# Optimization experiments

Hardware: AMD Instinct MI355X
Metric: run time of the kernel (lower is better)

Reference implementation:

```python
import jax, jax.numpy as jnp
import numpy as np

N_NODES = 50000
N_EDGES = 800000
D_IN = 128
D_OUT = 128


def setup_inputs() -> dict:
    key = jax.random.key(0)
    k1, k2, k3, k4, k5 = jax.random.split(key, 5)
    x = jax.random.normal(k1, (N_NODES, D_IN), dtype=jnp.float32)
    # fc weight, torch Linear convention: [out_dim, in_dim]
    W = jax.random.normal(k2, (D_OUT, D_IN), dtype=jnp.float32) * (1.0 / np.sqrt(D_IN))
    # attn_fc weight: [1, 2*out_dim], no bias
    a = jax.random.normal(k3, (1, 2 * D_OUT), dtype=jnp.float32) * (1.0 / np.sqrt(2 * D_OUT))
    src = jax.random.randint(k4, (N_EDGES,), 0, N_NODES)
    dst = jax.random.randint(k5, (N_EDGES,), 0, N_NODES)
    return {"x": x, "W": W, "a": a, "src": src, "dst": dst}


def reference(x, W, a, src, dst):
    # h = fc(x)
    h = x @ W.T  # [N, D_OUT]
    # attn_fc(cat([h_src, h_dst])) == h_src @ a[:D] + h_dst @ a[D:] (linear, no bias),
    # so precompute per-node scalars instead of materializing [E, 2*D_OUT].
    a_src = a[0, :D_OUT]
    a_dst = a[0, D_OUT:]
    s = h @ a_src  # [N]
    d = h @ a_dst  # [N]
    e = jax.nn.sigmoid(s[src] + d[dst])[:, None]  # [E, 1]
    msg = e * h[src]  # [E, D_OUT]  edge gather + weight
    # reduce: f[v] = sum over incoming edges of e * h_src
    f = jax.ops.segment_sum(msg, dst, num_segments=N_NODES)  # [N, D_OUT]
    return f
```

## Files before the change

### kernel.cpp

```cpp
#include <hip/hip_runtime.h>
#include <hip/hip_bf16.h>
#include <stdint.h>

#define NN 50000
#define NE 800000
#define DD 128
#define NBKT 3125
#define BCH 4096
#define BGRID ((NE + BCH - 1) / BCH)
#define CAP 384
#define SPILL_CAP 32768
#define GROWS 64
#define GGRID ((NN + GROWS - 1) / GROWS)
#define NSEG 4

typedef __attribute__((ext_vector_type(8))) unsigned short ushort8;
typedef __attribute__((ext_vector_type(8))) short short8;
typedef __attribute__((ext_vector_type(4))) float f32x4;

__device__ inline uint32_t cvtpk(float lo, float hi) {
    uint32_t r;
    asm("v_cvt_pk_bf16_f32 %0, %1, %2" : "=v"(r) : "v"(lo), "v"(hi));
    return r;
}
__device__ inline float bf_lo(uint32_t u) { return __uint_as_float(u << 16); }
__device__ inline float bf_hi(uint32_t u) { return __uint_as_float(u & 0xffff0000u); }

__global__ __launch_bounds__(256) void prep_k(const float* __restrict__ W,
                                              uint16_t* __restrict__ Wb,
                                              int* __restrict__ cntg) {
    int t = threadIdx.x;
    if (blockIdx.x < 13) {
        for (int k = blockIdx.x * 256 + t; k < NBKT + 4; k += 13 * 256) cntg[k] = 0;
    }
    int i = blockIdx.x * 256 + t;
    if (i < DD * DD) {
        uint32_t u = __float_as_uint(W[i]);
        Wb[i] = (uint16_t)((u + 0x7fffu + ((u >> 16) & 1u)) >> 16);
    }
}

__global__ __launch_bounds__(256) void fused_k(const float* __restrict__ x,
                                               const uint16_t* __restrict__ Wb,
                                               const float* __restrict__ a,
                                               const int* __restrict__ src,
                                               const int* __restrict__ dst,
                                               uint16_t* __restrict__ hb,
                                               float* __restrict__ sArr,
                                               float* __restrict__ dArr,
                                               int* __restrict__ cntg,
                                               int* __restrict__ scnt,
                                               uint32_t* __restrict__ rec,
                                               uint2* __restrict__ spill) {
    __shared__ int lh[NBKT];
    __shared__ int gb[NBKT];
    const int t = threadIdx.x;

    if ((int)blockIdx.x < GGRID) {
        const int l = t & 63, wid = t >> 6;
        const int r0 = blockIdx.x * GROWS;
        const int lr = l & 15, lk = l >> 4;

        f32x4 acc[8];
        #pragma unroll
        for (int c = 0; c < 8; ++c) acc[c] = f32x4{0.f, 0.f, 0.f, 0.f};

        const int arow = r0 + wid * 16 + lr;
        const int lrow = (arow < NN) ? arow : (NN - 1);
        const float* xp = x + (size_t)lrow * DD + lk * 8;

        #pragma unroll
        for (int kc = 0; kc < 4; ++kc) {
            float4 v0 = *(const float4*)(xp + kc * 32);
            float4 v1 = *(const float4*)(xp + kc * 32 + 4);
            union { uint32_t u[4]; short8 s; } A;
            A.u[0] = cvtpk(v0.x, v0.y); A.u[1] = cvtpk(v0.z, v0.w);
            A.u[2] = cvtpk(v1.x, v1.y); A.u[3] = cvtpk(v1.z, v1.w);
            #pragma unroll
            for (int c = 0; c < 8; ++c) {
                int col = c * 16 + lr;
                short8 bf_ = *(const short8*)(Wb + (size_t)col * DD + kc * 32 + lk * 8);
                acc[c] = __builtin_amdgcn_mfma_f32_16x16x32_bf16(A.s, bf_, acc[c], 0, 0, 0);
            }
        }

        float avs[8], avd[8];
        #pragma unroll
        for (int c = 0; c < 8; ++c) {
            avs[c] = a[c * 16 + lr];
            avd[c] = a[DD + c * 16 + lr];
        }
        #pragma unroll
        for (int i = 0; i < 4; ++i) {
            float ps = 0.f, pd = 0.f;
            #pragma unroll
            for (int c = 0; c < 8; ++c) {
                ps = fmaf(acc[c][i], avs[c], ps);
                pd = fmaf(acc[c][i], avd[c], pd);
            }
            #pragma unroll
            for (int o = 8; o > 0; o >>= 1) {
                ps += __shfl_xor(ps, o);
                pd += __shfl_xor(pd, o);
            }
            int row = r0 + wid * 16 + lk * 4 + i;
            if (lr == 0 && row < NN) { sArr[row] = ps; dArr[row] = pd; }
        }

        #pragma unroll
        for (int i = 0; i < 4; ++i) {
            int row = r0 + wid * 16 + lk * 4 + i;
            if (row < NN) {
                union { uint32_t u[4]; ushort8 s; } H;
                H.u[0] = cvtpk(acc[0][i], acc[1][i]);
                H.u[1] = cvtpk(acc[2][i], acc[3][i]);
                H.u[2] = cvtpk(acc[4][i], acc[5][i]);
                H.u[3] = cvtpk(acc[6][i], acc[7][i]);
                *(ushort8*)(hb + (size_t)row * DD + lr * 8) = H.s;
            }
        }
    } else {
        int bb = blockIdx.x - GGRID;
        for (int k = t; k < NBKT; k += 256) lh[k] = 0;
        __syncthreads();
        int base = bb * BCH;
        unsigned pk[16]; int bk[16];
        #pragma unroll
        for (int i = 0; i < 16; ++i) {
            int idx = base + i * 256 + t;
            if (idx < NE) {
                int s_ = src[idx], d_ = dst[idx];
                bk[i] = d_ >> 4;
                pk[i] = ((unsigned)(d_ & 15) << 16) | (unsigned)s_;
                atomicAdd(&lh[bk[i]], 1);
            } else bk[i] = -1;
        }
        __syncthreads();
        for (int k = t; k < NBKT; k += 256) {
            int c = lh[k];
            lh[k] = 0;
            gb[k] = c ? atomicAdd(&cntg[k], c) : 0;
        }
        __syncthreads();
        #pragma unroll
        for (int i = 0; i < 16; ++i) {
            if (bk[i] >= 0) {
                int sl = atomicAdd(&lh[bk[i]], 1);
                int p = gb[bk[i]] + sl;
                if (p < CAP) {
                    rec[(size_t)bk[i] * CAP + p] = pk[i];
                } else {
                    int sp = atomicAdd(scnt, 1);
                    if (sp < SPILL_CAP)
                        spill[sp] = make_uint2(pk[i] & 0xffffu,
                                               (unsigned)(bk[i] * 16 + (int)(pk[i] >> 16)));
                }
            }
        }
    }
}

__global__ __launch_bounds__(256) void bsort_agg_k(const uint16_t* __restrict__ hb,
                                                   const float* __restrict__ sA,
                                                   const float* __restrict__ dA,
                                                   const int* __restrict__ cntg,
                                                   const uint32_t* __restrict__ rec,
                                                   const int* __restrict__ scnt,
                                                   const uint2* __restrict__ spill,
                                                   float* __restrict__ out) {
    __shared__ uint32_t srt[CAP];
    __shared__ float    eL[CAP];
    __shared__ float dAl[16];
    __shared__ int hbin[NSEG * 16];
    __shared__ int soff[NSEG * 16 + 1];
    __shared__ int curw[NSEG * 16];
    int t = threadIdx.x, l = t & 63, wid = t >> 6;
    int b = blockIdx.x;
    int cnt = cntg[b]; if (cnt > CAP) cnt = CAP;
    int beg = b * CAP;
    int n0 = b * 16;
    int ns = *scnt; if (ns > SPILL_CAP) ns = SPILL_CAP;
    if (t < 64) hbin[t] = 0;
    if (t < 16) dAl[t] = dA[n0 + t];
    __syncthreads();

    uint32_t rc[2]; float er[2]; int bn[2]; int nrc = 0;
    for (int j = t; j < cnt; j += 256) {
        uint32_t r = rec[beg + j];
        int sv = (int)(r & 0xffffu);
        int sg = (sv >= 12500) + (sv >= 25000) + (sv >= 37500);
        int bin = (sg << 4) | (int)(r >> 16);
        rc[nrc] = r; bn[nrc] = bin;
        atomicAdd(&hbin[bin], 1);
        float z = sA[sv] + dAl[r >> 16];
        er[nrc] = 1.f / (1.f + __expf(-z));
        ++nrc;
    }
    __syncthreads();
    if (wid == 0) {
        int v = hbin[l];
        int inc = v;
        #pragma unroll
        for (int o = 1; o < 64; o <<= 1) {
            int nb = __shfl_up(inc, o);
            if (l >= o) inc += nb;
        }
        soff[l + 1] = inc;
        if (l == 0) soff[0] = 0;
        curw[l] = inc - v;
    }
    __syncthreads();
    for (int k = 0; k < nrc; ++k) {
        int p = atomicAdd(&curw[bn[k]], 1);
        srt[p] = rc[k];
        eL[p] = er[k];
    }
    __syncthreads();

    const int q = l >> 4, sl = l & 15;
    const int d = wid * 4 + q;
    const int n = n0 + d;
    const char* hbp = (const char*)hb;
    const int s0 = (blockIdx.x & 7) >> 1;
    float acc[8] = {0.f,0.f,0.f,0.f,0.f,0.f,0.f,0.f};

    #pragma unroll
    for (int so = 0; so < NSEG; ++so) {
        int s = (s0 + so) & (NSEG - 1);
        int bin = (s << 4) | d;
        int js = soff[bin], je = soff[bin + 1];
        for (int j = js; j < je; j += 2) {
            int j1 = j + 1;
            bool v1 = j1 < je;
            uint32_t r0 = srt[j];
            uint32_t r1 = srt[v1 ? j1 : j];
            float e0 = eL[j];
            float e1 = v1 ? eL[j1] : 0.f;
            uint4 u0 = *(const uint4*)(hbp + (size_t)(r0 & 0xffffu) * 256 + sl * 16);
            uint4 u1 = *(const uint4*)(hbp + (size_t)(r1 & 0xffffu) * 256 + sl * 16);
            acc[0] = fmaf(e0, bf_lo(u0.x), acc[0]); acc[1] = fmaf(e0, bf_hi(u0.x), acc[1]);
            acc[2] = fmaf(e0, bf_lo(u0.y), acc[2]); acc[3] = fmaf(e0, bf_hi(u0.y), acc[3]);
            acc[4] = fmaf(e0, bf_lo(u0.z), acc[4]); acc[5] = fmaf(e0, bf_hi(u0.z), acc[5]);
            acc[6] = fmaf(e0, bf_lo(u0.w), acc[6]); acc[7] = fmaf(e0, bf_hi(u0.w), acc[7]);
            acc[0] = fmaf(e1, bf_lo(u1.x), acc[0]); acc[1] = fmaf(e1, bf_hi(u1.x), acc[1]);
            acc[2] = fmaf(e1, bf_lo(u1.y), acc[2]); acc[3] = fmaf(e1, bf_hi(u1.y), acc[3]);
            acc[4] = fmaf(e1, bf_lo(u1.z), acc[4]); acc[5] = fmaf(e1, bf_hi(u1.z), acc[5]);
            acc[6] = fmaf(e1, bf_lo(u1.w), acc[6]); acc[7] = fmaf(e1, bf_hi(u1.w), acc[7]);
        }
    }

    if (ns > 0) {
        for (int i = 0; i < ns; ++i) {
            uint2 sp = spill[i];
            if ((int)sp.y == n) {
                float z = sA[sp.x] + dAl[d];
                float e = 1.f / (1.f + __expf(-z));
                uint4 u = *(const uint4*)(hbp + (size_t)sp.x * 256 + sl * 16);
                acc[0] = fmaf(e, bf_lo(u.x), acc[0]); acc[1] = fmaf(e, bf_hi(u.x), acc[1]);
                acc[2] = fmaf(e, bf_lo(u.y), acc[2]); acc[3] = fmaf(e, bf_hi(u.y), acc[3]);
                acc[4] = fmaf(e, bf_lo(u.z), acc[4]); acc[5] = fmaf(e, bf_hi(u.z), acc[5]);
                acc[6] = fmaf(e, bf_lo(u.w), acc[6]); acc[7] = fmaf(e, bf_hi(u.w), acc[7]);
            }
        }
    }

    float* orow = out + (size_t)n * DD;
    #pragma unroll
    for (int k = 0; k < 8; ++k) orow[k * 16 + sl] = acc[k];
}

__global__ __launch_bounds__(256) void edge_atomic_k(const int* __restrict__ src, const int* __restrict__ dst,
                                                     const float* __restrict__ sArr, const float* __restrict__ dArr,
                                                     const uint32_t* __restrict__ hb, float* __restrict__ out) {
    int wid = threadIdx.x >> 6, l = threadIdx.x & 63;
    int e = blockIdx.x * 4 + wid;
    if (e >= NE) return;
    int sv = src[e], dv = dst[e];
    float z = sArr[sv] + dArr[dv];
    float ev = 1.0f / (1.0f + __expf(-z));
    uint32_t u = hb[(size_t)sv * 64 + l];
    int colx = 32 * (l & 3) + (l >> 2);
    atomicAdd(&out[(size_t)dv * DD + colx],      ev * bf_lo(u));
    atomicAdd(&out[(size_t)dv * DD + colx + 16], ev * bf_hi(u));
}

extern "C" void kernel_launch(void* const* d_in, const int* in_sizes, int n_in,
                              void* d_out, int out_size, void* d_ws, size_t ws_size,
                              hipStream_t stream) {
    const float* x  = (const float*)d_in[0];
    const float* W  = (const float*)d_in[1];
    const float* a  = (const float*)d_in[2];
    const int* src  = (const int*)d_in[3];
    const int* dst  = (const int*)d_in[4];
    float* out = (float*)d_out;

    char* p = (char*)d_ws;
    uint16_t* hb = (uint16_t*)p;            p += (size_t)NN * DD * 2;
    uint16_t* Wb = (uint16_t*)p;            p += (size_t)DD * DD * 2;
    float* sA    = (float*)p;               p += (size_t)NN * 4;
    float* dA    = (float*)p;               p += (size_t)NN * 4;
    int*   cntg  = (int*)p;                 p += (size_t)NBKT * 4;
    int*   scnt  = (int*)p;                 p += 16;
    uint32_t* rec = (uint32_t*)(((uintptr_t)p + 15) & ~(uintptr_t)15);
    p = (char*)(rec + (size_t)NBKT * CAP);
    uint2* spill = (uint2*)p;               p += (size_t)SPILL_CAP * 8;
    size_t need  = (size_t)(p - (char*)d_ws);

    if (ws_size >= need) {
        prep_k<<<64, 256, 0, stream>>>(W, Wb, cntg);
        fused_k<<<GGRID + BGRID, 256, 0, stream>>>(x, Wb, a, src, dst,
                                                   hb, sA, dA, cntg, scnt, rec, spill);
        bsort_agg_k<<<NBKT, 256, 0, stream>>>(hb, sA, dA, cntg, rec, scnt, spill, out);
    } else {
        hipMemsetAsync(out, 0, sizeof(float) * (size_t)NN * DD, stream);
        prep_k<<<64, 256, 0, stream>>>(W, Wb, cntg);
        fused_k<<<GGRID, 256, 0, stream>>>(x, Wb, a, src, dst,
                                           hb, sA, dA, cntg, scnt, rec, spill);
        edge_atomic_k<<<NE / 4, 256, 0, stream>>>(src, dst, sA, dA, (const uint32_t*)hb, out);
    }
}
```

Measured before the change: 71.55 us.

## Spread each node's edges across lane groups and reduce partial sums with shuffles

The aggregation kernel drops the 4-way source-segment binning, so edges are now sorted only by destination node. Each 16-lane group handling a node splits into four 4-lane subgroups, and each subgroup processes different edges. Every lane loads 64-byte chunks of the row in four passes into separate accumulators, and xor-shuffles then combine the subgroups' partial sums. This is meant to put more independent gathers in flight per node and to cut the serial loop length on high-degree nodes. In exchange it uses more registers (32 accumulators), does extra shuffle work, and the lane-to-column mapping becomes more complex, which may hurt coalescing and cache locality.

```diff
diff --git a/kernel.cpp b/kernel.cpp
--- a/kernel.cpp
+++ b/kernel.cpp
@@ -12,7 +12,6 @@
 #define SPILL_CAP 32768
 #define GROWS 64
 #define GGRID ((NN + GROWS - 1) / GROWS)
-#define NSEG 4
 
 typedef __attribute__((ext_vector_type(8))) unsigned short ushort8;
 typedef __attribute__((ext_vector_type(8))) short short8;
@@ -171,83 +170,95 @@
     __shared__ uint32_t srt[CAP];
     __shared__ float    eL[CAP];
     __shared__ float dAl[16];
-    __shared__ int hbin[NSEG * 16];
-    __shared__ int soff[NSEG * 16 + 1];
-    __shared__ int curw[NSEG * 16];
+    __shared__ int h16[16];
+    __shared__ int s17[17];
+    __shared__ int curw[16];
     int t = threadIdx.x, l = t & 63, wid = t >> 6;
     int b = blockIdx.x;
     int cnt = cntg[b]; if (cnt > CAP) cnt = CAP;
     int beg = b * CAP;
     int n0 = b * 16;
     int ns = *scnt; if (ns > SPILL_CAP) ns = SPILL_CAP;
-    if (t < 64) hbin[t] = 0;
-    if (t < 16) dAl[t] = dA[n0 + t];
+    if (t < 16) { h16[t] = 0; dAl[t] = dA[n0 + t]; }
     __syncthreads();
 
-    uint32_t rc[2]; float er[2]; int bn[2]; int nrc = 0;
+    uint32_t rc[2]; float er[2]; int nrc = 0;
     for (int j = t; j < cnt; j += 256) {
         uint32_t r = rec[beg + j];
-        int sv = (int)(r & 0xffffu);
-        int sg = (sv >= 12500) + (sv >= 25000) + (sv >= 37500);
-        int bin = (sg << 4) | (int)(r >> 16);
-        rc[nrc] = r; bn[nrc] = bin;
-        atomicAdd(&hbin[bin], 1);
-        float z = sA[sv] + dAl[r >> 16];
+        rc[nrc] = r;
+        atomicAdd(&h16[r >> 16], 1);
+        float z = sA[r & 0xffffu] + dAl[r >> 16];
         er[nrc] = 1.f / (1.f + __expf(-z));
         ++nrc;
     }
     __syncthreads();
     if (wid == 0) {
-        int v = hbin[l];
+        int v = (l < 16) ? h16[l] : 0;
         int inc = v;
         #pragma unroll
-        for (int o = 1; o < 64; o <<= 1) {
+        for (int o = 1; o < 16; o <<= 1) {
             int nb = __shfl_up(inc, o);
             if (l >= o) inc += nb;
         }
-        soff[l + 1] = inc;
-        if (l == 0) soff[0] = 0;
-        curw[l] = inc - v;
+        if (l < 16) { s17[l + 1] = inc; curw[l] = inc - v; }
+        if (l == 0) s17[0] = 0;
     }
     __syncthreads();
     for (int k = 0; k < nrc; ++k) {
-        int p = atomicAdd(&curw[bn[k]], 1);
-        srt[p] = rc[k];
+        uint32_t r = rc[k];
+        int p = atomicAdd(&curw[r >> 16], 1);
+        srt[p] = r;
         eL[p] = er[k];
     }
     __syncthreads();
 
     const int q = l >> 4, sl = l & 15;
+    const int ep = sl >> 2;
+    const int bo = (sl & 3) * 16;
     const int d = wid * 4 + q;
     const int n = n0 + d;
     const char* hbp = (const char*)hb;
-    const int s0 = (blockIdx.x & 7) >> 1;
-    float acc[8] = {0.f,0.f,0.f,0.f,0.f,0.f,0.f,0.f};
-
-    #pragma unroll
-    for (int so = 0; so < NSEG; ++so) {
-        int s = (s0 + so) & (NSEG - 1);
-        int bin = (s << 4) | d;
-        int js = soff[bin], je = soff[bin + 1];
-        for (int j = js; j < je; j += 2) {
-            int j1 = j + 1;
-            bool v1 = j1 < je;
-            uint32_t r0 = srt[j];
-            uint32_t r1 = srt[v1 ? j1 : j];
-            float e0 = eL[j];
+    const int js = s17[d], je = s17[d + 1];
+    float acc[4][8];
+    #pragma unroll
+    for (int p = 0; p < 4; ++p)
+        #pragma unroll
+        for (int k = 0; k < 8; ++k) acc[p][k] = 0.f;
+
+    #pragma unroll
+    for (int p = 0; p < 4; ++p) {
+        const size_t po = (size_t)(p * 64 + bo);
+        for (int j = js; j < je; j += 8) {
+            int j0 = j + ep, j1 = j + 4 + ep;
+            bool v0 = j0 < je, v1 = j1 < je;
+            uint32_t r0 = srt[v0 ? j0 : js];
+            uint32_t r1 = srt[v1 ? j1 : js];
+            float e0 = v0 ? eL[j0] : 0.f;
             float e1 = v1 ? eL[j1] : 0.f;
-            uint4 u0 = *(const uint4*)(hbp + (size_t)(r0 & 0xffffu) * 256 + sl * 16);
-            uint4 u1 = *(const uint4*)(hbp + (size_t)(r1 & 0xffffu) * 256 + sl * 16);
-            acc[0] = fmaf(e0, bf_lo(u0.x), acc[0]); acc[1] = fmaf(e0, bf_hi(u0.x), acc[1]);
-            acc[2] = fmaf(e0, bf_lo(u0.y), acc[2]); acc[3] = fmaf(e0, bf_hi(u0.y), acc[3]);
-            acc[4] = fmaf(e0, bf_lo(u0.z), acc[4]); acc[5] = fmaf(e0, bf_hi(u0.z), acc[5]);
-            acc[6] = fmaf(e0, bf_lo(u0.w), acc[6]); acc[7] = fmaf(e0, bf_hi(u0.w), acc[7]);
-            acc[0] = fmaf(e1, bf_lo(u1.x), acc[0]); acc[1] = fmaf(e1, bf_hi(u1.x), acc[1]);
-            acc[2] = fmaf(e1, bf_lo(u1.y), acc[2]); acc[3] = fmaf(e1, bf_hi(u1.y), acc[3]);
-            acc[4] = fmaf(e1, bf_lo(u1.z), acc[4]); acc[5] = fmaf(e1, bf_hi(u1.z), acc[5]);
-            acc[6] = fmaf(e1, bf_lo(u1.w), acc[6]); acc[7] = fmaf(e1, bf_hi(u1.w), acc[7]);
-        }
-    }
+            uint4 u0 = *(const uint4*)(hbp + (size_t)(r0 & 0xffffu) * 256 + po);
+            uint4 u1 = *(const uint4*)(hbp + (size_t)(r1 & 0xffffu) * 256 + po);
+            acc[p][0] = fmaf(e0, bf_lo(u0.x), acc[p][0]); acc[p][1] = fmaf(e0, bf_hi(u0.x), acc[p][1]);
+            acc[p][2] = fmaf(e0, bf_lo(u0.y), acc[p][2]); acc[p][3] = fmaf(e0, bf_hi(u0.y), acc[p][3]);
+            acc[p][4] = fmaf(e0, bf_lo(u0.z), acc[p][4]); acc[p][5] = fmaf(e0, bf_hi(u0.z), acc[p][5]);
+            acc[p][6] = fmaf(e0, bf_lo(u0.w), acc[p][6]); acc[p][7] = fmaf(e0, bf_hi(u0.w), acc[p][7]);
+            acc[p][0] = fmaf(e1, bf_lo(u1.x), acc[p][0]); acc[p][1] = fmaf(e1, bf_hi(u1.x), acc[p][1]);
+            acc[p][2] = fmaf(e1, bf_lo(u1.y), acc[p][2]); acc[p][3] = fmaf(e1, bf_hi(u1.y), acc[p][3]);
+            acc[p][4] = fmaf(e1, bf_lo(u1.z), acc[p][4]); acc[p][5] = fmaf(e1, bf_hi(u1.z), acc[p][5]);
+            acc[p][6] = fmaf(e1, bf_lo(u1.w), acc[p][6]); acc[p][7] = fmaf(e1, bf_hi(u1.w), acc[p][7]);
+        }
+    }
+
+    #pragma unroll
+    for (int p = 0; p < 4; ++p)
+        #pragma unroll
+        for (int k = 0; k < 8; ++k) {
+            acc[p][k] += __shfl_xor(acc[p][k], 4);
+            acc[p][k] += __shfl_xor(acc[p][k], 8);
+        }
+    float v[8];
+    #pragma unroll
+    for (int k = 0; k < 8; ++k)
+        v[k] = (ep == 0) ? acc[0][k] : (ep == 1) ? acc[1][k] : (ep == 2) ? acc[2][k] : acc[3][k];
 
     if (ns > 0) {
         for (int i = 0; i < ns; ++i) {
@@ -256,17 +267,17 @@
                 float z = sA[sp.x] + dAl[d];
                 float e = 1.f / (1.f + __expf(-z));
                 uint4 u = *(const uint4*)(hbp + (size_t)sp.x * 256 + sl * 16);
-                acc[0] = fmaf(e, bf_lo(u.x), acc[0]); acc[1] = fmaf(e, bf_hi(u.x), acc[1]);
-                acc[2] = fmaf(e, bf_lo(u.y), acc[2]); acc[3] = fmaf(e, bf_hi(u.y), acc[3]);
-                acc[4] = fmaf(e, bf_lo(u.z), acc[4]); acc[5] = fmaf(e, bf_hi(u.z), acc[5]);
-                acc[6] = fmaf(e, bf_lo(u.w), acc[6]); acc[7] = fmaf(e, bf_hi(u.w), acc[7]);
+                v[0] = fmaf(e, bf_lo(u.x), v[0]); v[1] = fmaf(e, bf_hi(u.x), v[1]);
+                v[2] = fmaf(e, bf_lo(u.y), v[2]); v[3] = fmaf(e, bf_hi(u.y), v[3]);
+                v[4] = fmaf(e, bf_lo(u.z), v[4]); v[5] = fmaf(e, bf_hi(u.z), v[5]);
+                v[6] = fmaf(e, bf_lo(u.w), v[6]); v[7] = fmaf(e, bf_hi(u.w), v[7]);
             }
         }
     }
 
     float* orow = out + (size_t)n * DD;
     #pragma unroll
-    for (int k = 0; k < 8; ++k) orow[k * 16 + sl] = acc[k];
+    for (int k = 0; k < 8; ++k) orow[k * 16 + sl] = v[k];
 }
 
 __global__ __launch_bounds__(256) void edge_atomic_k(const int* __restrict__ src, const int* __restrict__ dst,
```

Result: slower. 86.29 us (+20.6%).
